# Kernel tuning notes

Hardware: AMD Instinct MI355X
Metric: run time of the kernel (lower is better)

The kernel has to match this reference:

```python
import jax, jax.numpy as jnp
import numpy as np

HIDDEN = 4096
NUM_HEADS = 32
HEAD_DIM = 128
NUM_KV_HEADS = 8
KV_GROUPS = NUM_HEADS // NUM_KV_HEADS
ROPE_THETA = 10000.0
SEQ = 2048
BATCH = 1
NEG_INF = -1e9


def fake_quant_int8(x):
    """Per-tensor symmetric int8 fake quantization (absmax scale)."""
    scale = jnp.maximum(jnp.max(jnp.abs(x)) / 127.0, 1e-8)
    q = jnp.clip(jnp.round(x / scale), -127.0, 127.0) * scale
    # straight-through estimator (no-op in fwd-only, keeps code shared)
    return x + jax.lax.stop_gradient(q - x)


def rotate_half(x):
    x1, x2 = jnp.split(x, 2, axis=-1)
    return jnp.concatenate([-x2, x1], axis=-1)


def rope_cos_sin(position_ids):
    inv_freq = 1.0 / (ROPE_THETA ** (jnp.arange(0, HEAD_DIM, 2, dtype=jnp.float32) / HEAD_DIM))
    freqs = position_ids.astype(jnp.float32)[..., None] * inv_freq  # [B,S,HD/2]
    emb = jnp.concatenate([freqs, freqs], axis=-1)                  # [B,S,HD]
    return jnp.cos(emb), jnp.sin(emb)


def setup_inputs() -> dict:
    key = jax.random.key(0)
    k1, k2, k3, k4, k5 = jax.random.split(key, 5)
    hidden_states = jax.random.normal(k1, (BATCH, SEQ, HIDDEN), dtype=jnp.float32)
    causal = jnp.tril(jnp.ones((SEQ, SEQ), dtype=bool))
    attention_mask = jnp.where(causal, 0.0, NEG_INF).astype(jnp.float32)[None, None]  # [1,1,S,S]
    position_ids = jnp.arange(SEQ, dtype=jnp.int64 if jax.config.jax_enable_x64 else jnp.int32)[None, :]
    s = 0.02
    wq = jax.random.normal(k2, (NUM_HEADS * HEAD_DIM, HIDDEN), dtype=jnp.float32) * s
    wk = jax.random.normal(k3, (NUM_KV_HEADS * HEAD_DIM, HIDDEN), dtype=jnp.float32) * s
    wv = jax.random.normal(k4, (NUM_KV_HEADS * HEAD_DIM, HIDDEN), dtype=jnp.float32) * s
    wo = jax.random.normal(k5, (HIDDEN, NUM_HEADS * HEAD_DIM), dtype=jnp.float32) * s
    return {"hidden_states": hidden_states, "attention_mask": attention_mask,
            "position_ids": position_ids, "wq": wq, "wk": wk, "wv": wv, "wo": wo}


def reference(hidden_states, attention_mask, position_ids, wq, wk, wv, wo):
    B, S, _ = hidden_states.shape

    def qlinear(x, w):  # quantized linear: fake-quant act and weight, y = x @ w.T
        return fake_quant_int8(x) @ fake_quant_int8(w).T

    q = qlinear(hidden_states, wq).reshape(B, S, NUM_HEADS, HEAD_DIM).transpose(0, 2, 1, 3)
    k = qlinear(hidden_states, wk).reshape(B, S, NUM_KV_HEADS, HEAD_DIM).transpose(0, 2, 1, 3)
    v = qlinear(hidden_states, wv).reshape(B, S, NUM_KV_HEADS, HEAD_DIM).transpose(0, 2, 1, 3)

    cos, sin = rope_cos_sin(position_ids)      # [B,S,HD]
    cos, sin = cos[:, None], sin[:, None]      # [B,1,S,HD]
    q = q * cos + rotate_half(q) * sin
    k = k * cos + rotate_half(k) * sin

    # repeat_kv: GQA -> full heads
    k = jnp.repeat(k, KV_GROUPS, axis=1)
    v = jnp.repeat(v, KV_GROUPS, axis=1)

    # quantized QK^T
    scores = jnp.einsum('bhqd,bhkd->bhqk', fake_quant_int8(q), fake_quant_int8(k))
    scores = scores * (1.0 / np.sqrt(HEAD_DIM).astype(np.float32))
    scores = scores + attention_mask[:, :, :, :S]
    probs = jax.nn.softmax(scores.astype(jnp.float32), axis=-1).astype(q.dtype)
    # attention_dropout = 0.0 -> identity

    # quantized AV
    attn_out = jnp.einsum('bhqk,bhkd->bhqd', fake_quant_int8(probs), fake_quant_int8(v))
    attn_out = attn_out.transpose(0, 2, 1, 3).reshape(B, S, NUM_HEADS * HEAD_DIM)
    return qlinear(attn_out, wo)
```

## Files before the change

### kernel.cpp

```cpp
#include <hip/hip_runtime.h>
#include <stdint.h>

#define SEQ   2048
#define HID   4096
#define NH    32
#define NKV   8
#define KVDIM 1024
#define KVCAT 2048

typedef int v4i __attribute__((ext_vector_type(4)));

#define VMCNT0 asm volatile("s_waitcnt vmcnt(0)" ::: "memory")

__device__ __forceinline__ void gload16(const void* g, void* l) {
    __builtin_amdgcn_global_load_lds(
        (const __attribute__((address_space(1))) void*)(uintptr_t)g,
        (__attribute__((address_space(3))) void*)(uintptr_t)l, 16, 0, 0);
}

__device__ __forceinline__ float slot_scale(const unsigned* slots, int slot) {
    return fmaxf(__uint_as_float(slots[slot << 5]) / 127.0f, 1e-8f);
}

__device__ __forceinline__ int q8v(float x, float s) {
    int v = (int)rintf(x / s);
    return v < -127 ? -127 : (v > 127 ? 127 : v);
}

__device__ __forceinline__ float fexp2(float x) {
    float r; asm("v_exp_f32 %0, %1" : "=v"(r) : "v"(x)); return r;
}

__device__ __forceinline__ float amax4(const float* __restrict__ p, long v) {
    float4 x = *(const float4*)(p + v * 4);
    return fmaxf(fmaxf(fabsf(x.x), fabsf(x.y)), fmaxf(fabsf(x.z), fabsf(x.w)));
}

__device__ __forceinline__ void block_amax_store(float m, float* part) {
    __shared__ float sm[4];
    int lane = threadIdx.x & 63, w = threadIdx.x >> 6;
    for (int off = 32; off; off >>= 1) m = fmaxf(m, __shfl_xor(m, off, 64));
    if (lane == 0) sm[w] = m;
    __syncthreads();
    if (threadIdx.x == 0)
        part[blockIdx.x] = fmaxf(fmaxf(sm[0], sm[1]), fmaxf(sm[2], sm[3]));
}

#define NV0 ((long)SEQ * HID / 4)
#define NV1 ((long)HID * HID / 4)
#define NV2 ((long)KVDIM * HID / 4)
__global__ void k_absmax5(const float* __restrict__ a0, const float* __restrict__ a1,
                          const float* __restrict__ a2, const float* __restrict__ a3,
                          const float* __restrict__ a4, float* __restrict__ part) {
    int b = blockIdx.x;
    const float* p; long n; int lb, nb;
    if (b < 342)       { p = a0; n = NV0; lb = b;        nb = 342; }
    else if (b < 1025) { p = a1; n = NV1; lb = b - 342;  nb = 683; }
    else if (b < 1196) { p = a2; n = NV2; lb = b - 1025; nb = 171; }
    else if (b < 1367) { p = a3; n = NV2; lb = b - 1196; nb = 171; }
    else               { p = a4; n = NV1; lb = b - 1367; nb = 681; }
    long str = (long)nb * 256;
    float mm[8] = {0.f, 0.f, 0.f, 0.f, 0.f, 0.f, 0.f, 0.f};
    long v = (long)lb * 256 + threadIdx.x;
    for (; v + 7 * str < n; v += 8 * str) {
        #pragma unroll
        for (int j = 0; j < 8; j++) mm[j] = fmaxf(mm[j], amax4(p, v + j * str));
    }
    for (; v < n; v += str) mm[0] = fmaxf(mm[0], amax4(p, v));
    float m = fmaxf(fmaxf(fmaxf(mm[0], mm[1]), fmaxf(mm[2], mm[3])),
                    fmaxf(fmaxf(mm[4], mm[5]), fmaxf(mm[6], mm[7])));
    block_amax_store(m, part);
}

__global__ void k_reduceA(const float* __restrict__ part, unsigned* slots) {
    __shared__ float sm[4];
    const int lo[5] = {0, 342, 1025, 1196, 1367};
    const int hi[5] = {342, 1025, 1196, 1367, 2048};
    int t = threadIdx.x, lane = t & 63, w = t >> 6;
    for (int s = 0; s < 5; s++) {
        float m = 0.f;
        for (int i = lo[s] + t; i < hi[s]; i += 256) m = fmaxf(m, part[i]);
        for (int off = 32; off; off >>= 1) m = fmaxf(m, __shfl_xor(m, off, 64));
        if (lane == 0) sm[w] = m;
        __syncthreads();
        if (t == 0)
            slots[s << 5] = __float_as_uint(fmaxf(fmaxf(sm[0], sm[1]), fmaxf(sm[2], sm[3])));
        __syncthreads();
    }
}

__global__ void k_reduceB(const float* __restrict__ p1, const float* __restrict__ p2,
                          const float* __restrict__ p3, unsigned* slots) {
    __shared__ float sm[4];
    int t = threadIdx.x, lane = t & 63, w = t >> 6;
    const float* ps[3] = {p1, p2, p3};
    const int cnt[3] = {2048, 1024, 256};
    const int sl[3] = {5, 6, 7};
    for (int s = 0; s < 3; s++) {
        float m = 0.f;
        for (int i = t; i < cnt[s]; i += 256) m = fmaxf(m, ps[s][i]);
        for (int off = 32; off; off >>= 1) m = fmaxf(m, __shfl_xor(m, off, 64));
        if (lane == 0) sm[w] = m;
        __syncthreads();
        if (t == 0)
            slots[sl[s] << 5] = __float_as_uint(fmaxf(fmaxf(sm[0], sm[1]), fmaxf(sm[2], sm[3])));
        __syncthreads();
    }
}

__device__ __forceinline__ void qstore4(const float* __restrict__ src, long v,
                                        int8_t* __restrict__ dst, float s) {
    float4 x = *(const float4*)(src + v * 4);
    unsigned pa = (unsigned)(uint8_t)(int8_t)q8v(x.x, s)
                | ((unsigned)(uint8_t)(int8_t)q8v(x.y, s) << 8)
                | ((unsigned)(uint8_t)(int8_t)q8v(x.z, s) << 16)
                | ((unsigned)(uint8_t)(int8_t)q8v(x.w, s) << 24);
    *(unsigned*)(dst + v * 4) = pa;
}

__global__ void k_quant4(const float* __restrict__ a0, const float* __restrict__ a1,
                         const float* __restrict__ a2, const float* __restrict__ a3,
                         int8_t* __restrict__ d0, int8_t* __restrict__ d1,
                         int8_t* __restrict__ d2, int8_t* __restrict__ d3,
                         const unsigned* __restrict__ slots) {
    int b = blockIdx.x;
    const float* p; int8_t* d; long n; int slot, lb, nb;
    if (b < 512)       { p = a0; d = d0; n = NV0; slot = 0; lb = b;        nb = 512; }
    else if (b < 1536) { p = a1; d = d1; n = NV1; slot = 1; lb = b - 512;  nb = 1024; }
    else if (b < 1792) { p = a2; d = d2; n = NV2; slot = 2; lb = b - 1536; nb = 256; }
    else               { p = a3; d = d3; n = NV2; slot = 3; lb = b - 1792; nb = 256; }
    float s = slot_scale(slots, slot);
    long str = (long)nb * 256;
    long v = (long)lb * 256 + threadIdx.x;
    for (; v + 3 * str < n; v += 4 * str) {
        #pragma unroll
        for (int j = 0; j < 4; j++) qstore4(p, v + j * str, d, s);
    }
    for (; v < n; v += str) qstore4(p, v, d, s);
}

__global__ void k_quant(const float* __restrict__ x, int8_t* __restrict__ q, long nvec,
                        int rshift, long cmaskv, long ld,
                        const unsigned* __restrict__ slots, int slot) {
    float s = slot_scale(slots, slot);
    long gs = (long)gridDim.x * blockDim.x;
    long v = blockIdx.x * (long)blockDim.x + threadIdx.x;
    for (; v + 3 * gs < nvec; v += 4 * gs) {
        #pragma unroll
        for (int j = 0; j < 4; j++) {
            long vid = v + j * gs;
            long r = vid >> rshift;
            long c = (vid & cmaskv) << 2;
            float4 vv = *(const float4*)(x + r * ld + c);
            unsigned pa = (unsigned)(uint8_t)(int8_t)q8v(vv.x, s)
                        | ((unsigned)(uint8_t)(int8_t)q8v(vv.y, s) << 8)
                        | ((unsigned)(uint8_t)(int8_t)q8v(vv.z, s) << 16)
                        | ((unsigned)(uint8_t)(int8_t)q8v(vv.w, s) << 24);
            *(unsigned*)(q + vid * 4) = pa;
        }
    }
    for (; v < nvec; v += gs) {
        long r = v >> rshift;
        long c = (v & cmaskv) << 2;
        float4 vv = *(const float4*)(x + r * ld + c);
        unsigned pa = (unsigned)(uint8_t)(int8_t)q8v(vv.x, s)
                    | ((unsigned)(uint8_t)(int8_t)q8v(vv.y, s) << 8)
                    | ((unsigned)(uint8_t)(int8_t)q8v(vv.z, s) << 16)
                    | ((unsigned)(uint8_t)(int8_t)q8v(vv.w, s) << 24);
        *(unsigned*)(q + v * 4) = pa;
    }
}

__global__ void k_ropetab(const int* __restrict__ pos, float* __restrict__ ct,
                          float* __restrict__ st) {
    int tid = blockIdx.x * blockDim.x + threadIdx.x;
    if (tid >= SEQ * 64) return;
    int i = tid & 63, s = tid >> 6;
    double inv = 1.0 / pow(10000.0, (double)((float)(2 * i) * (1.0f / 128.0f)));
    float invf = (float)inv;
    float angf = (float)pos[s] * invf;
    double a = (double)angf;
    ct[tid] = (float)cos(a);
    st[tid] = (float)sin(a);
}

__global__ void k_rope(float* __restrict__ x, long ld, int hbits, int total,
                       const float* __restrict__ ct, const float* __restrict__ st,
                       float* __restrict__ part) {
    float m = 0.f;
    for (int t = blockIdx.x * blockDim.x + threadIdx.x; t < total;
         t += gridDim.x * blockDim.x) {
        int i4 = t & 15;
        int h = (t >> 4) & ((1 << hbits) - 1);
        int s = t >> (4 + hbits);
        long base = (long)s * ld + h * 128 + i4 * 4;
        float4 a = *(float4*)(x + base);
        float4 b = *(float4*)(x + base + 64);
        float4 c = *(const float4*)(ct + s * 64 + i4 * 4);
        float4 sn = *(const float4*)(st + s * 64 + i4 * 4);
        float4 o0, o1;
        o0.x = a.x * c.x - b.x * sn.x;  o1.x = b.x * c.x + a.x * sn.x;
        o0.y = a.y * c.y - b.y * sn.y;  o1.y = b.y * c.y + a.y * sn.y;
        o0.z = a.z * c.z - b.z * sn.z;  o1.z = b.z * c.z + a.z * sn.z;
        o0.w = a.w * c.w - b.w * sn.w;  o1.w = b.w * c.w + a.w * sn.w;
        *(float4*)(x + base) = o0;
        *(float4*)(x + base + 64) = o1;
        m = fmaxf(m,
            fmaxf(fmaxf(fmaxf(fabsf(o0.x), fabsf(o0.y)), fmaxf(fabsf(o0.z), fabsf(o0.w))),
                  fmaxf(fmaxf(fabsf(o1.x), fabsf(o1.y)), fmaxf(fabsf(o1.z), fabsf(o1.w)))));
    }
    block_amax_store(m, part);
}

__global__ void k_transq(const float* __restrict__ src, long lds_, int8_t* __restrict__ dst,
                         long ldd, const unsigned* __restrict__ slots, int slot) {
    __shared__ float t[32][33];
    float s = slot_scale(slots, slot);
    int bx = blockIdx.x, by = blockIdx.y;
    int tid = threadIdx.x;
    int c = tid & 31, r0 = tid >> 5;
    #pragma unroll
    for (int j = 0; j < 4; j++) {
        int r = r0 + j * 8;
        t[r][c] = src[(long)(by * 32 + r) * lds_ + bx * 32 + c];
    }
    __syncthreads();
    int d = tid >> 3, k4 = (tid & 7) * 4;
    unsigned pa = 0;
    #pragma unroll
    for (int j = 0; j < 4; j++) {
        int iv = q8v(t[k4 + j][d], s);
        pa |= ((unsigned)(uint8_t)(int8_t)iv) << (8 * j);
    }
    *(unsigned*)(dst + (long)(bx * 32 + d) * ldd + by * 32 + k4) = pa;
}

__global__ __launch_bounds__(256) void k_gemm_i8(
    const int8_t* __restrict__ A, const int8_t* __restrict__ B, float* __restrict__ C,
    int M, int N, int K, unsigned* slots,
    int slotA, int slotB, int slotB2, int nsplit, float* am_part, int am_col0) {
    __shared__ int8_t As[2][128 * 128];
    __shared__ int8_t Bs[2][128 * 128];
    const v4i vzero = {0, 0, 0, 0};
    int tid = threadIdx.x, lane = tid & 63, wid = tid >> 6;
    int nbx = N >> 7;
    int nwg = gridDim.x, wg = blockIdx.x;
    int cpx = nwg >> 3;
    int swz = (wg & 7) * cpx + (wg >> 3);
    int bm = swz / nbx, bn = swz % nbx;
    long rowA0 = (long)bm * 128, colB0 = (long)bn * 128;
    int wrow = (wid >> 1) * 64, wcol = (wid & 1) * 64;
    int lr = lane >> 3;
    int swc = ((lane & 7) ^ lr) * 16;
    const int8_t* ga = A + (rowA0 + wid * 8 + lr) * (long)K + swc;
    const int8_t* gb = B + (colB0 + wid * 8 + lr) * (long)K + swc;
    v4i acc[4][4];
    #pragma unroll
    for (int m = 0; m < 4; m++)
        #pragma unroll
        for (int n = 0; n < 4; n++) acc[m][n] = vzero;

    auto STAGE = [&](int buf, int kt) {
        #pragma unroll
        for (int i = 0; i < 4; i++) {
            gload16(ga + kt + (long)(i * 32) * K, &As[buf][(wid * 8 + i * 32) * 128]);
            gload16(gb + kt + (long)(i * 32) * K, &Bs[buf][(wid * 8 + i * 32) * 128]);
        }
    };
    auto COMPUTE = [&](int buf) {
        #pragma unroll
        for (int ks = 0; ks < 2; ks++) {
            v4i af[4], bf[4];
            #pragma unroll
            for (int m = 0; m < 4; m++) {
                int row = wrow + m * 16 + (lane & 15);
                af[m] = *(const v4i*)(&As[buf][row * 128 + (((ks * 4 + (lane >> 4)) ^ (row & 7)) * 16)]);
            }
            #pragma unroll
            for (int n = 0; n < 4; n++) {
                int row = wcol + n * 16 + (lane & 15);
                bf[n] = *(const v4i*)(&Bs[buf][row * 128 + (((ks * 4 + (lane >> 4)) ^ (row & 7)) * 16)]);
            }
            #pragma unroll
            for (int m = 0; m < 4; m++)
                #pragma unroll
                for (int n = 0; n < 4; n++)
                    acc[m][n] = __builtin_amdgcn_mfma_i32_16x16x64_i8(af[m], bf[n], acc[m][n], 0, 0, 0);
        }
    };

    STAGE(0, 0);
    VMCNT0;
    __syncthreads();
    int nt = K >> 7, cur = 0;
    for (int t = 0; t < nt - 1; t++) {
        STAGE(cur ^ 1, (t + 1) << 7);
        COMPUTE(cur);
        VMCNT0;
        __syncthreads();
        cur ^= 1;
    }
    COMPUTE(cur);

    float sA = slot_scale(slots, slotA);
    float sB1 = slot_scale(slots, slotB);
    float sB2 = slot_scale(slots, slotB2);
    float am = 0.f;
    #pragma unroll
    for (int m = 0; m < 4; m++) {
        long row0 = rowA0 + wrow + m * 16 + ((lane >> 4) << 2);
        #pragma unroll
        for (int n = 0; n < 4; n++) {
            int col = (int)colB0 + wcol + n * 16 + (lane & 15);
            float sc = sA * ((col < nsplit) ? sB1 : sB2);
            float* cp = C + row0 * N + col;
            #pragma unroll
            for (int r = 0; r < 4; r++) {
                float val = sc * (float)acc[m][n][r];
                cp[(long)r * N] = val;
                if (col >= am_col0) am = fmaxf(am, fabsf(val));
            }
        }
    }
    if (am_part) block_amax_store(am, am_part);
}

__global__ __launch_bounds__(256) void k_attn(
    const int8_t* __restrict__ Qq, const int8_t* __restrict__ Kq, const int8_t* __restrict__ Vtq,
    int* __restrict__ AO, unsigned* slots) {
    __shared__ int8_t Qs[64 * 128];
    __shared__ int8_t Ks[2][64 * 128];
    __shared__ int8_t Vs[2][128 * 64];
    __shared__ int smx[4];
    const v4i vzero = {0, 0, 0, 0};
    const int NEGS = -(1 << 29);
    int tid = threadIdx.x, lane = tid & 63, w = tid >> 6;
    int qlan = lane & 15, g = lane >> 4;
    int idx = blockIdx.x;
    int qb = 31 - (idx >> 5), h = idx & 31, kvh = h >> 2;
    float sq = slot_scale(slots, 5), sk = slot_scale(slots, 6);
    float c2 = sq * sk * 0.08838834764831845f * 1.4426950408889634f;
    int lr8 = lane >> 3;
    int swc = ((lane & 7) ^ lr8) * 16;
    int lr4 = lane >> 2;
    int vswc = ((lane & 3) ^ (lr4 & 3)) * 16;
    const int8_t* kbase = Kq + ((long)(w * 8 + lr8)) * KVDIM + kvh * 128 + swc;
    const int8_t* vbase = Vtq + ((long)kvh * 128 + w * 16 + lr4) * SEQ + vswc;
    auto STAGE_K = [&](int buf, int kt) {
        #pragma unroll
        for (int i = 0; i < 2; i++)
            gload16(kbase + ((long)kt * 64 + i * 32) * KVDIM, &Ks[buf][(w * 8 + i * 32) * 128]);
    };
    auto STAGE_V = [&](int buf, int kt) {
        #pragma unroll
        for (int i = 0; i < 2; i++)
            gload16(vbase + (long)(i * 64) * SEQ + kt * 64, &Vs[buf][(w * 16 + i * 64) * 64]);
    };
    {
        const int8_t* qbase = Qq + ((long)qb * 64 + w * 8 + lr8) * HID + h * 128 + swc;
        #pragma unroll
        for (int i = 0; i < 2; i++)
            gload16(qbase + (long)(i * 32) * HID, &Qs[(w * 8 + i * 32) * 128]);
    }
    STAGE_K(0, 0);
    VMCNT0;
    __syncthreads();
    v4i aq[2];
    #pragma unroll
    for (int ks = 0; ks < 2; ks++) {
        int row = w * 16 + qlan;
        aq[ks] = *(const v4i*)(&Qs[row * 128 + (((ks * 4 + g) ^ (row & 7)) * 16)]);
    }
    int mi = -(1 << 30);
    float l = 0.f;
    int buf = 0;
    for (int kt = 0; kt <= qb; kt++) {
        if (kt < qb) STAGE_K(buf ^ 1, kt + 1);
        v4i sf[4] = {vzero, vzero, vzero, vzero};
        __builtin_amdgcn_s_setprio(1);
        #pragma unroll
        for (int ks = 0; ks < 2; ks++)
            #pragma unroll
            for (int f = 0; f < 4; f++) {
                int row = f * 16 + qlan;
                v4i bk = *(const v4i*)(&Ks[buf][row * 128 + (((ks * 4 + g) ^ (row & 7)) * 16)]);
                sf[f] = __builtin_amdgcn_mfma_i32_16x16x64_i8(bk, aq[ks], sf[f], 0, 0, 0);
            }
        __builtin_amdgcn_s_setprio(0);
        int sv[16];
        if (kt == qb) {
            int qthr = w * 16 + qlan;
            #pragma unroll
            for (int f = 0; f < 4; f++)
                #pragma unroll
                for (int r = 0; r < 4; r++) {
                    int kl = f * 16 + g * 4 + r;
                    sv[f * 4 + r] = (kl > qthr) ? NEGS : sf[f][r];
                }
        } else {
            #pragma unroll
            for (int f = 0; f < 4; f++)
                #pragma unroll
                for (int r = 0; r < 4; r++) sv[f * 4 + r] = sf[f][r];
        }
        int tm = sv[0];
        #pragma unroll
        for (int e = 1; e < 16; e++) tm = tm > sv[e] ? tm : sv[e];
        tm = max(tm, __shfl_xor(tm, 16, 64));
        tm = max(tm, __shfl_xor(tm, 32, 64));
        int mn = tm > mi ? tm : mi;
        float esc = fexp2(c2 * (float)(mi - mn));
        float es = 0.f;
        #pragma unroll
        for (int e = 0; e < 16; e++) es += fexp2(c2 * (float)(sv[e] - mn));
        es += __shfl_xor(es, 16, 64);
        es += __shfl_xor(es, 32, 64);
        l = l * esc + es;
        mi = mn;
        VMCNT0;
        __syncthreads();
        buf ^= 1;
    }
    float invl = 127.0f / l;
    unsigned* Ps32 = (unsigned*)Qs;
    int pwr = w * 320;
    v4i of[8];
    #pragma unroll
    for (int nf = 0; nf < 8; nf++) of[nf] = vzero;
    STAGE_K(0, 0);
    STAGE_V(0, 0);
    VMCNT0;
    __syncthreads();
    buf = 0;
    for (int kt = 0; kt <= qb; kt++) {
        if (kt < qb) { STAGE_K(buf ^ 1, kt + 1); STAGE_V(buf ^ 1, kt + 1); }
        v4i sf[4] = {vzero, vzero, vzero, vzero};
        __builtin_amdgcn_s_setprio(1);
        #pragma unroll
        for (int ks = 0; ks < 2; ks++)
            #pragma unroll
            for (int f = 0; f < 4; f++) {
                int row = f * 16 + qlan;
                v4i bk = *(const v4i*)(&Ks[buf][row * 128 + (((ks * 4 + g) ^ (row & 7)) * 16)]);
                sf[f] = __builtin_amdgcn_mfma_i32_16x16x64_i8(bk, aq[ks], sf[f], 0, 0, 0);
            }
        __builtin_amdgcn_s_setprio(0);
        if (kt == qb) {
            int qthr = w * 16 + qlan;
            #pragma unroll
            for (int f = 0; f < 4; f++) {
                unsigned pk = 0;
                #pragma unroll
                for (int r = 0; r < 4; r++) {
                    int kl = f * 16 + g * 4 + r;
                    int s = (kl > qthr) ? NEGS : sf[f][r];
                    float t = fexp2(c2 * (float)(s - mi));
                    int pq = (int)rintf(t * invl);
                    pk |= ((unsigned)pq) << (8 * r);
                }
                Ps32[pwr + (4 * f + g) * 20 + qlan] = pk;
            }
        } else {
            #pragma unroll
            for (int f = 0; f < 4; f++) {
                unsigned pk = 0;
                #pragma unroll
                for (int r = 0; r < 4; r++) {
                    float t = fexp2(c2 * (float)(sf[f][r] - mi));
                    int pq = (int)rintf(t * invl);
                    pk |= ((unsigned)pq) << (8 * r);
                }
                Ps32[pwr + (4 * f + g) * 20 + qlan] = pk;
            }
        }
        int rb = pwr + 80 * g + qlan;
        v4i ap;
        ap[0] = (int)Ps32[rb];
        ap[1] = (int)Ps32[rb + 20];
        ap[2] = (int)Ps32[rb + 40];
        ap[3] = (int)Ps32[rb + 60];
        __builtin_amdgcn_s_setprio(1);
        #pragma unroll
        for (int nf = 0; nf < 8; nf++) {
            int row = nf * 16 + qlan;
            v4i bv = *(const v4i*)(&Vs[buf][row * 64 + ((g ^ (row & 3)) * 16)]);
            of[nf] = __builtin_amdgcn_mfma_i32_16x16x64_i8(ap, bv, of[nf], 0, 0, 0);
        }
        __builtin_amdgcn_s_setprio(0);
        VMCNT0;
        __syncthreads();
        buf ^= 1;
    }
    int mymax = 0;
    #pragma unroll
    for (int nf = 0; nf < 8; nf++)
        #pragma unroll
        for (int r = 0; r < 4; r++) {
            int val = of[nf][r];
            int av = val < 0 ? -val : val;
            mymax = av > mymax ? av : mymax;
            int qg = qb * 64 + w * 16 + 4 * g + r;
            AO[(long)qg * HID + h * 128 + nf * 16 + qlan] = val;
        }
    #pragma unroll
    for (int off = 1; off < 64; off <<= 1) {
        int o2 = __shfl_xor(mymax, off, 64);
        mymax = o2 > mymax ? o2 : mymax;
    }
    if (lane == 0) smx[w] = mymax;
    __syncthreads();
    if (tid == 0) {
        int mm = max(max(smx[0], smx[1]), max(smx[2], smx[3]));
        atomicMax(slots + (8 << 5), (unsigned)mm);
    }
}

__global__ void k_quant_ao(const int* __restrict__ a, int8_t* __restrict__ q, unsigned* slots) {
    float sv = slot_scale(slots, 7);
    float spv = (1.0f / 127.0f) * sv;
    float amax = spv * (float)(int)slots[8 << 5];
    float s = fmaxf(amax / 127.0f, 1e-8f);
    long nvec = (long)SEQ * HID / 4;
    long gs = (long)gridDim.x * blockDim.x;
    long v = blockIdx.x * (long)blockDim.x + threadIdx.x;
    for (; v + 3 * gs < nvec; v += 4 * gs) {
        #pragma unroll
        for (int j = 0; j < 4; j++) {
            long vid = v + j * gs;
            int4 x = *(const int4*)(a + vid * 4);
            int a0 = q8v(spv * (float)x.x, s);
            int a1 = q8v(spv * (float)x.y, s);
            int a2 = q8v(spv * (float)x.z, s);
            int a3 = q8v(spv * (float)x.w, s);
            unsigned pa = (unsigned)(uint8_t)(int8_t)a0
                        | ((unsigned)(uint8_t)(int8_t)a1 << 8)
                        | ((unsigned)(uint8_t)(int8_t)a2 << 16)
                        | ((unsigned)(uint8_t)(int8_t)a3 << 24);
            *(unsigned*)(q + vid * 4) = pa;
        }
    }
    for (; v < nvec; v += gs) {
        int4 x = *(const int4*)(a + v * 4);
        int a0 = q8v(spv * (float)x.x, s);
        int a1 = q8v(spv * (float)x.y, s);
        int a2 = q8v(spv * (float)x.z, s);
        int a3 = q8v(spv * (float)x.w, s);
        unsigned pa = (unsigned)(uint8_t)(int8_t)a0
                    | ((unsigned)(uint8_t)(int8_t)a1 << 8)
                    | ((unsigned)(uint8_t)(int8_t)a2 << 16)
                    | ((unsigned)(uint8_t)(int8_t)a3 << 24);
        *(unsigned*)(q + v * 4) = pa;
    }
    if (blockIdx.x == 0 && threadIdx.x == 0) slots[9 << 5] = __float_as_uint(amax);
}

extern "C" void kernel_launch(void* const* d_in, const int* in_sizes, int n_in,
                              void* d_out, int out_size, void* d_ws, size_t ws_size,
                              hipStream_t stream) {
    (void)in_sizes; (void)n_in; (void)out_size;
    const float* hid = (const float*)d_in[0];
    const int* pos = (const int*)d_in[2];
    const float* wqp = (const float*)d_in[3];
    const float* wkp = (const float*)d_in[4];
    const float* wvp = (const float*)d_in[5];
    const float* wop = (const float*)d_in[6];
    float* out = (float*)d_out;
    char* ws = (char*)d_ws;

    size_t o = 0;
    auto alloc = [&](size_t sz) { size_t r = o; o += (sz + 255) & ~(size_t)255; return r; };
    unsigned* slots = (unsigned*)(ws + alloc(2048));
    float* P0 = (float*)(ws + alloc(2048 * 4));
    float* P1 = (float*)(ws + alloc(2048 * 4));
    float* P2 = (float*)(ws + alloc(1024 * 4));
    float* P3 = (float*)(ws + alloc(256 * 4));
    int8_t* Xq   = (int8_t*)(ws + alloc((size_t)SEQ * HID));
    int8_t* Wqq  = (int8_t*)(ws + alloc((size_t)HID * HID));
    int8_t* Wkvq = (int8_t*)(ws + alloc((size_t)KVCAT * HID));
    float*  Qf   = (float*)(ws + alloc((size_t)SEQ * HID * 4));
    float*  KVf  = (float*)(ws + alloc((size_t)SEQ * KVCAT * 4));
    int8_t* Qq   = (int8_t*)(ws + alloc((size_t)SEQ * HID));
    int8_t* Kq   = (int8_t*)(ws + alloc((size_t)SEQ * KVDIM));
    int8_t* Vtq  = (int8_t*)(ws + alloc((size_t)KVDIM * SEQ));
    float*  ctab = (float*)(ws + alloc((size_t)SEQ * 64 * 4));
    float*  stab = (float*)(ws + alloc((size_t)SEQ * 64 * 4));
    if (ws_size < o) return;
    int8_t* Woq = Wqq;
    int*    AOint = (int*)Qf;
    int8_t* AOq = Xq;

    hipMemsetAsync(slots, 0, 2048, stream);
    k_ropetab<<<SEQ * 64 / 256, 256, 0, stream>>>(pos, ctab, stab);
    k_absmax5<<<2048, 256, 0, stream>>>(hid, wqp, wkp, wvp, wop, P0);
    k_reduceA<<<1, 256, 0, stream>>>(P0, slots);
    k_quant4<<<2048, 256, 0, stream>>>(hid, wqp, wkp, wvp,
                                       Xq, Wqq, Wkvq, Wkvq + (size_t)KVDIM * HID, slots);
    k_gemm_i8<<<512, 256, 0, stream>>>(Xq, Wqq, Qf, SEQ, HID, HID, slots,
                                       0, 1, 1, 1 << 30, nullptr, 1 << 30);
    k_gemm_i8<<<256, 256, 0, stream>>>(Xq, Wkvq, KVf, SEQ, KVCAT, HID, slots,
                                       0, 2, 3, KVDIM, P3, KVDIM);
    const long CALL = 0x3FFFFFFFL;
    k_quant<<<2048, 256, 0, stream>>>(wop, Woq, (long)HID * HID / 4, 40, CALL, 0, slots, 4);
    k_rope<<<2048, 256, 0, stream>>>(Qf, HID, 5, SEQ * NH * 16, ctab, stab, P1);
    k_rope<<<1024, 256, 0, stream>>>(KVf, KVCAT, 3, SEQ * NKV * 16, ctab, stab, P2);
    k_reduceB<<<1, 256, 0, stream>>>(P1, P2, P3, slots);
    k_quant<<<2048, 256, 0, stream>>>(Qf, Qq, (long)SEQ * HID / 4, 40, CALL, 0, slots, 5);
    k_quant<<<512, 256, 0, stream>>>(KVf, Kq, (long)SEQ * KVDIM / 4, 8, 255, KVCAT, slots, 6);
    k_transq<<<dim3(32, 64), 256, 0, stream>>>(KVf + KVDIM, KVCAT, Vtq, SEQ, slots, 7);
    k_attn<<<1024, 256, 0, stream>>>(Qq, Kq, Vtq, AOint, slots);
    k_quant_ao<<<2048, 256, 0, stream>>>(AOint, AOq, slots);
    k_gemm_i8<<<512, 256, 0, stream>>>(AOq, Woq, out, SEQ, HID, HID, slots,
                                       9, 4, 4, 1 << 30, nullptr, 1 << 30);
}
```

Measured before the change: 312.6 us.

## Fuse RoPE and absmax into GEMM epilogue, restage absmax and attention loads

The RoPE rotation and its absmax partials now run inside the Q and KV GEMM epilogues through an LDS exchange buffer, which removes the two standalone k_rope passes over Qf and KVf. The absmax kernel now stages 16 KB chunks into LDS with global_load_lds double buffering and writes per-tensor partials. The attention kernel drops its double-buffered LDS K/V and instead prefetches the next tile into registers, adding two barriers per iteration. This frees LDS, but it risks exposing load latency and adding sync cost inside attention.

```diff
diff --git a/kernel.cpp b/kernel.cpp
--- a/kernel.cpp
+++ b/kernel.cpp
@@ -31,59 +31,66 @@
     float r; asm("v_exp_f32 %0, %1" : "=v"(r) : "v"(x)); return r;
 }
 
-__device__ __forceinline__ float amax4(const float* __restrict__ p, long v) {
-    float4 x = *(const float4*)(p + v * 4);
-    return fmaxf(fmaxf(fabsf(x.x), fabsf(x.y)), fmaxf(fabsf(x.z), fabsf(x.w)));
-}
-
-__device__ __forceinline__ void block_amax_store(float m, float* part) {
+__device__ __forceinline__ void block_amax_part(float m, float* dst) {
     __shared__ float sm[4];
     int lane = threadIdx.x & 63, w = threadIdx.x >> 6;
     for (int off = 32; off; off >>= 1) m = fmaxf(m, __shfl_xor(m, off, 64));
     if (lane == 0) sm[w] = m;
     __syncthreads();
     if (threadIdx.x == 0)
-        part[blockIdx.x] = fmaxf(fmaxf(sm[0], sm[1]), fmaxf(sm[2], sm[3]));
-}
-
-#define NV0 ((long)SEQ * HID / 4)
-#define NV1 ((long)HID * HID / 4)
-#define NV2 ((long)KVDIM * HID / 4)
-__global__ void k_absmax5(const float* __restrict__ a0, const float* __restrict__ a1,
-                          const float* __restrict__ a2, const float* __restrict__ a3,
-                          const float* __restrict__ a4, float* __restrict__ part) {
-    int b = blockIdx.x;
-    const float* p; long n; int lb, nb;
-    if (b < 342)       { p = a0; n = NV0; lb = b;        nb = 342; }
-    else if (b < 1025) { p = a1; n = NV1; lb = b - 342;  nb = 683; }
-    else if (b < 1196) { p = a2; n = NV2; lb = b - 1025; nb = 171; }
-    else if (b < 1367) { p = a3; n = NV2; lb = b - 1196; nb = 171; }
-    else               { p = a4; n = NV1; lb = b - 1367; nb = 681; }
-    long str = (long)nb * 256;
-    float mm[8] = {0.f, 0.f, 0.f, 0.f, 0.f, 0.f, 0.f, 0.f};
-    long v = (long)lb * 256 + threadIdx.x;
-    for (; v + 7 * str < n; v += 8 * str) {
-        #pragma unroll
-        for (int j = 0; j < 8; j++) mm[j] = fmaxf(mm[j], amax4(p, v + j * str));
-    }
-    for (; v < n; v += str) mm[0] = fmaxf(mm[0], amax4(p, v));
-    float m = fmaxf(fmaxf(fmaxf(mm[0], mm[1]), fmaxf(mm[2], mm[3])),
-                    fmaxf(fmaxf(mm[4], mm[5]), fmaxf(mm[6], mm[7])));
-    block_amax_store(m, part);
+        *dst = fmaxf(fmaxf(sm[0], sm[1]), fmaxf(sm[2], sm[3]));
+    __syncthreads();
+}
+
+__global__ __launch_bounds__(256) void k_absmax5(
+    const float* __restrict__ a0, const float* __restrict__ a1,
+    const float* __restrict__ a2, const float* __restrict__ a3,
+    const float* __restrict__ a4, float* __restrict__ part) {
+    __shared__ int8_t SB[4][2][4096];
+    int lane = threadIdx.x & 63, w = threadIdx.x >> 6;
+    const char* bases[5] = {(const char*)a0, (const char*)a1, (const char*)a2,
+                            (const char*)a3, (const char*)a4};
+    const int lo[5] = {0, 2048, 6144, 7168, 8192};
+    float m[5] = {0.f, 0.f, 0.f, 0.f, 0.f};
+    int u0 = blockIdx.x * 12;
+    auto tensor_of = [&](int u) {
+        return (u < 2048) ? 0 : (u < 6144) ? 1 : (u < 7168) ? 2 : (u < 8192) ? 3 : 4; };
+    auto stage = [&](int u, int buf) {
+        int t = tensor_of(u);
+        const char* s = bases[t] + ((long)(u - lo[t]) << 14) + w * 4096 + lane * 16;
+        #pragma unroll
+        for (int i = 0; i < 4; i++) gload16(s + i * 1024, &SB[w][buf][i * 1024]);
+    };
+    stage(u0, 0);
+    for (int j = 0; j < 12; j++) {
+        if (j < 11) {
+            stage(u0 + j + 1, (j + 1) & 1);
+            asm volatile("s_waitcnt vmcnt(4)" ::: "memory");
+        } else {
+            asm volatile("s_waitcnt vmcnt(0)" ::: "memory");
+        }
+        int t = tensor_of(u0 + j);
+        #pragma unroll
+        for (int i = 0; i < 4; i++) {
+            float4 v = *(const float4*)&SB[w][j & 1][i * 1024 + lane * 16];
+            m[t] = fmaxf(m[t],
+                fmaxf(fmaxf(fabsf(v.x), fabsf(v.y)), fmaxf(fabsf(v.z), fabsf(v.w))));
+        }
+    }
+    __syncthreads();
+    for (int t = 0; t < 5; t++) block_amax_part(m[t], part + t * 1024 + blockIdx.x);
 }
 
 __global__ void k_reduceA(const float* __restrict__ part, unsigned* slots) {
     __shared__ float sm[4];
-    const int lo[5] = {0, 342, 1025, 1196, 1367};
-    const int hi[5] = {342, 1025, 1196, 1367, 2048};
-    int t = threadIdx.x, lane = t & 63, w = t >> 6;
+    int t0 = threadIdx.x, lane = t0 & 63, w = t0 >> 6;
     for (int s = 0; s < 5; s++) {
         float m = 0.f;
-        for (int i = lo[s] + t; i < hi[s]; i += 256) m = fmaxf(m, part[i]);
+        for (int i = t0; i < 1024; i += 256) m = fmaxf(m, part[s * 1024 + i]);
         for (int off = 32; off; off >>= 1) m = fmaxf(m, __shfl_xor(m, off, 64));
         if (lane == 0) sm[w] = m;
         __syncthreads();
-        if (t == 0)
+        if (t0 == 0)
             slots[s << 5] = __float_as_uint(fmaxf(fmaxf(sm[0], sm[1]), fmaxf(sm[2], sm[3])));
         __syncthreads();
     }
@@ -92,17 +99,17 @@
 __global__ void k_reduceB(const float* __restrict__ p1, const float* __restrict__ p2,
                           const float* __restrict__ p3, unsigned* slots) {
     __shared__ float sm[4];
-    int t = threadIdx.x, lane = t & 63, w = t >> 6;
+    int t0 = threadIdx.x, lane = t0 & 63, w = t0 >> 6;
     const float* ps[3] = {p1, p2, p3};
-    const int cnt[3] = {2048, 1024, 256};
+    const int cnt[3] = {512, 128, 128};
     const int sl[3] = {5, 6, 7};
     for (int s = 0; s < 3; s++) {
         float m = 0.f;
-        for (int i = t; i < cnt[s]; i += 256) m = fmaxf(m, ps[s][i]);
+        for (int i = t0; i < cnt[s]; i += 256) m = fmaxf(m, ps[s][i]);
         for (int off = 32; off; off >>= 1) m = fmaxf(m, __shfl_xor(m, off, 64));
         if (lane == 0) sm[w] = m;
         __syncthreads();
-        if (t == 0)
+        if (t0 == 0)
             slots[sl[s] << 5] = __float_as_uint(fmaxf(fmaxf(sm[0], sm[1]), fmaxf(sm[2], sm[3])));
         __syncthreads();
     }
@@ -118,6 +125,9 @@
     *(unsigned*)(dst + v * 4) = pa;
 }
 
+#define NV0 ((long)SEQ * HID / 4)
+#define NV1 ((long)HID * HID / 4)
+#define NV2 ((long)KVDIM * HID / 4)
 __global__ void k_quant4(const float* __restrict__ a0, const float* __restrict__ a1,
                          const float* __restrict__ a2, const float* __restrict__ a3,
                          int8_t* __restrict__ d0, int8_t* __restrict__ d1,
@@ -184,34 +194,6 @@
     st[tid] = (float)sin(a);
 }
 
-__global__ void k_rope(float* __restrict__ x, long ld, int hbits, int total,
-                       const float* __restrict__ ct, const float* __restrict__ st,
-                       float* __restrict__ part) {
-    float m = 0.f;
-    for (int t = blockIdx.x * blockDim.x + threadIdx.x; t < total;
-         t += gridDim.x * blockDim.x) {
-        int i4 = t & 15;
-        int h = (t >> 4) & ((1 << hbits) - 1);
-        int s = t >> (4 + hbits);
-        long base = (long)s * ld + h * 128 + i4 * 4;
-        float4 a = *(float4*)(x + base);
-        float4 b = *(float4*)(x + base + 64);
-        float4 c = *(const float4*)(ct + s * 64 + i4 * 4);
-        float4 sn = *(const float4*)(st + s * 64 + i4 * 4);
-        float4 o0, o1;
-        o0.x = a.x * c.x - b.x * sn.x;  o1.x = b.x * c.x + a.x * sn.x;
-        o0.y = a.y * c.y - b.y * sn.y;  o1.y = b.y * c.y + a.y * sn.y;
-        o0.z = a.z * c.z - b.z * sn.z;  o1.z = b.z * c.z + a.z * sn.z;
-        o0.w = a.w * c.w - b.w * sn.w;  o1.w = b.w * c.w + a.w * sn.w;
-        *(float4*)(x + base) = o0;
-        *(float4*)(x + base + 64) = o1;
-        m = fmaxf(m,
-            fmaxf(fmaxf(fmaxf(fabsf(o0.x), fabsf(o0.y)), fmaxf(fabsf(o0.z), fabsf(o0.w))),
-                  fmaxf(fmaxf(fabsf(o1.x), fabsf(o1.y)), fmaxf(fabsf(o1.z), fabsf(o1.w)))));
-    }
-    block_amax_store(m, part);
-}
-
 __global__ void k_transq(const float* __restrict__ src, long lds_, int8_t* __restrict__ dst,
                          long ldd, const unsigned* __restrict__ slots, int slot) {
     __shared__ float t[32][33];
@@ -238,9 +220,12 @@
 __global__ __launch_bounds__(256) void k_gemm_i8(
     const int8_t* __restrict__ A, const int8_t* __restrict__ B, float* __restrict__ C,
     int M, int N, int K, unsigned* slots,
-    int slotA, int slotB, int slotB2, int nsplit, float* am_part, int am_col0) {
-    __shared__ int8_t As[2][128 * 128];
-    __shared__ int8_t Bs[2][128 * 128];
+    int slotA, int slotB, int slotB2, int nsplit,
+    float* pQ, float* pK, float* pV, int ropemode,
+    const float* __restrict__ ct, const float* __restrict__ st) {
+    __shared__ int8_t POOL[65536];
+    int8_t (*As)[16384] = (int8_t(*)[16384])POOL;
+    int8_t (*Bs)[16384] = (int8_t(*)[16384])(POOL + 32768);
     const v4i vzero = {0, 0, 0, 0};
     int tid = threadIdx.x, lane = tid & 63, wid = tid >> 6;
     int nbx = N >> 7;
@@ -305,32 +290,83 @@
     float sA = slot_scale(slots, slotA);
     float sB1 = slot_scale(slots, slotB);
     float sB2 = slot_scale(slots, slotB2);
-    float am = 0.f;
-    #pragma unroll
-    for (int m = 0; m < 4; m++) {
-        long row0 = rowA0 + wrow + m * 16 + ((lane >> 4) << 2);
-        #pragma unroll
-        for (int n = 0; n < 4; n++) {
-            int col = (int)colB0 + wcol + n * 16 + (lane & 15);
-            float sc = sA * ((col < nsplit) ? sB1 : sB2);
-            float* cp = C + row0 * N + col;
-            #pragma unroll
-            for (int r = 0; r < 4; r++) {
-                float val = sc * (float)acc[m][n][r];
-                cp[(long)r * N] = val;
-                if (col >= am_col0) am = fmaxf(am, fabsf(val));
-            }
-        }
-    }
-    if (am_part) block_amax_store(am, am_part);
+    int qc = lane & 15, rgrp = (lane >> 4) << 2;
+    if (ropemode == 1 || (ropemode == 2 && bn < 8)) {
+        __syncthreads();
+        float* EX = (float*)POOL;
+        #pragma unroll
+        for (int m = 0; m < 4; m++)
+            #pragma unroll
+            for (int n = 0; n < 4; n++) {
+                int coll = wcol + n * 16 + qc;
+                #pragma unroll
+                for (int r = 0; r < 4; r++) {
+                    int rowl = wrow + m * 16 + rgrp + r;
+                    EX[rowl * 128 + (coll ^ ((rowl & 1) << 4))] = sA * sB1 * (float)acc[m][n][r];
+                }
+            }
+        __syncthreads();
+        float am = 0.f;
+        #pragma unroll
+        for (int m = 0; m < 4; m++)
+            #pragma unroll
+            for (int n = 0; n < 4; n++) {
+                int coll = wcol + n * 16 + qc;
+                #pragma unroll
+                for (int r = 0; r < 4; r++) {
+                    int rowl = wrow + m * 16 + rgrp + r;
+                    long srow = rowA0 + rowl;
+                    float self = EX[rowl * 128 + (coll ^ ((rowl & 1) << 4))];
+                    float pv = EX[rowl * 128 + ((coll ^ 64) ^ ((rowl & 1) << 4))];
+                    float c = ct[srow * 64 + (coll & 63)];
+                    float sn = st[srow * 64 + (coll & 63)];
+                    float o = (coll < 64) ? self * c - pv * sn : self * c + pv * sn;
+                    am = fmaxf(am, fabsf(o));
+                    C[srow * N + colB0 + coll] = o;
+                }
+            }
+        block_amax_part(am, (ropemode == 1) ? pQ + blockIdx.x : pK + bm * 8 + (bn & 7));
+    } else if (ropemode == 2) {
+        float am = 0.f;
+        #pragma unroll
+        for (int m = 0; m < 4; m++) {
+            long row0 = rowA0 + wrow + m * 16 + rgrp;
+            #pragma unroll
+            for (int n = 0; n < 4; n++) {
+                int col = (int)colB0 + wcol + n * 16 + qc;
+                float sc = sA * ((col < nsplit) ? sB1 : sB2);
+                float* cp = C + row0 * N + col;
+                #pragma unroll
+                for (int r = 0; r < 4; r++) {
+                    float val = sc * (float)acc[m][n][r];
+                    cp[(long)r * N] = val;
+                    am = fmaxf(am, fabsf(val));
+                }
+            }
+        }
+        block_amax_part(am, pV + bm * 8 + (bn & 7));
+    } else {
+        #pragma unroll
+        for (int m = 0; m < 4; m++) {
+            long row0 = rowA0 + wrow + m * 16 + rgrp;
+            #pragma unroll
+            for (int n = 0; n < 4; n++) {
+                int col = (int)colB0 + wcol + n * 16 + qc;
+                float sc = sA * ((col < nsplit) ? sB1 : sB2);
+                float* cp = C + row0 * N + col;
+                #pragma unroll
+                for (int r = 0; r < 4; r++) cp[(long)r * N] = sc * (float)acc[m][n][r];
+            }
+        }
+    }
 }
 
 __global__ __launch_bounds__(256) void k_attn(
     const int8_t* __restrict__ Qq, const int8_t* __restrict__ Kq, const int8_t* __restrict__ Vtq,
     int* __restrict__ AO, unsigned* slots) {
     __shared__ int8_t Qs[64 * 128];
-    __shared__ int8_t Ks[2][64 * 128];
-    __shared__ int8_t Vs[2][128 * 64];
+    __shared__ int8_t Ks[64 * 128];
+    __shared__ int8_t Vs[128 * 64];
     __shared__ int smx[4];
     const v4i vzero = {0, 0, 0, 0};
     const int NEGS = -(1 << 29);
@@ -346,23 +382,22 @@
     int vswc = ((lane & 3) ^ (lr4 & 3)) * 16;
     const int8_t* kbase = Kq + ((long)(w * 8 + lr8)) * KVDIM + kvh * 128 + swc;
     const int8_t* vbase = Vtq + ((long)kvh * 128 + w * 16 + lr4) * SEQ + vswc;
-    auto STAGE_K = [&](int buf, int kt) {
-        #pragma unroll
-        for (int i = 0; i < 2; i++)
-            gload16(kbase + ((long)kt * 64 + i * 32) * KVDIM, &Ks[buf][(w * 8 + i * 32) * 128]);
+    int kds0 = (w * 8) * 128 + lane * 16,  kds1 = (w * 8 + 32) * 128 + lane * 16;
+    int vds0 = (w * 16) * 64 + lane * 16,  vds1 = (w * 16 + 64) * 64 + lane * 16;
+    auto STAGE_K_g = [&](int kt) {
+        gload16(kbase + ((long)kt * 64) * KVDIM, &Ks[(w * 8) * 128]);
+        gload16(kbase + ((long)kt * 64 + 32) * KVDIM, &Ks[(w * 8 + 32) * 128]);
     };
-    auto STAGE_V = [&](int buf, int kt) {
-        #pragma unroll
-        for (int i = 0; i < 2; i++)
-            gload16(vbase + (long)(i * 64) * SEQ + kt * 64, &Vs[buf][(w * 16 + i * 64) * 64]);
+    auto STAGE_V_g = [&](int kt) {
+        gload16(vbase + kt * 64, &Vs[(w * 16) * 64]);
+        gload16(vbase + (long)64 * SEQ + kt * 64, &Vs[(w * 16 + 64) * 64]);
     };
     {
         const int8_t* qbase = Qq + ((long)qb * 64 + w * 8 + lr8) * HID + h * 128 + swc;
-        #pragma unroll
-        for (int i = 0; i < 2; i++)
-            gload16(qbase + (long)(i * 32) * HID, &Qs[(w * 8 + i * 32) * 128]);
-    }
-    STAGE_K(0, 0);
+        gload16(qbase, &Qs[(w * 8) * 128]);
+        gload16(qbase + (long)32 * HID, &Qs[(w * 8 + 32) * 128]);
+    }
+    STAGE_K_g(0);
     VMCNT0;
     __syncthreads();
     v4i aq[2];
@@ -373,9 +408,13 @@
     }
     int mi = -(1 << 30);
     float l = 0.f;
-    int buf = 0;
     for (int kt = 0; kt <= qb; kt++) {
-        if (kt < qb) STAGE_K(buf ^ 1, kt + 1);
+        bool pf = kt < qb;
+        v4i kr0, kr1;
+        if (pf) {
+            kr0 = *(const v4i*)(kbase + ((long)(kt + 1) * 64) * KVDIM);
+            kr1 = *(const v4i*)(kbase + ((long)(kt + 1) * 64 + 32) * KVDIM);
+        }
         v4i sf[4] = {vzero, vzero, vzero, vzero};
         __builtin_amdgcn_s_setprio(1);
         #pragma unroll
@@ -383,7 +422,7 @@
             #pragma unroll
             for (int f = 0; f < 4; f++) {
                 int row = f * 16 + qlan;
-                v4i bk = *(const v4i*)(&Ks[buf][row * 128 + (((ks * 4 + g) ^ (row & 7)) * 16)]);
+                v4i bk = *(const v4i*)(&Ks[row * 128 + (((ks * 4 + g) ^ (row & 7)) * 16)]);
                 sf[f] = __builtin_amdgcn_mfma_i32_16x16x64_i8(bk, aq[ks], sf[f], 0, 0, 0);
             }
         __builtin_amdgcn_s_setprio(0);
@@ -417,9 +456,12 @@
         es += __shfl_xor(es, 32, 64);
         l = l * esc + es;
         mi = mn;
-        VMCNT0;
-        __syncthreads();
-        buf ^= 1;
+        if (pf) {
+            __syncthreads();
+            *(v4i*)&Ks[kds0] = kr0;
+            *(v4i*)&Ks[kds1] = kr1;
+            __syncthreads();
+        }
     }
     float invl = 127.0f / l;
     unsigned* Ps32 = (unsigned*)Qs;
@@ -427,13 +469,20 @@
     v4i of[8];
     #pragma unroll
     for (int nf = 0; nf < 8; nf++) of[nf] = vzero;
-    STAGE_K(0, 0);
-    STAGE_V(0, 0);
+    __syncthreads();
+    STAGE_K_g(0);
+    STAGE_V_g(0);
     VMCNT0;
     __syncthreads();
-    buf = 0;
     for (int kt = 0; kt <= qb; kt++) {
-        if (kt < qb) { STAGE_K(buf ^ 1, kt + 1); STAGE_V(buf ^ 1, kt + 1); }
+        bool pf = kt < qb;
+        v4i kr0, kr1, vr0, vr1;
+        if (pf) {
+            kr0 = *(const v4i*)(kbase + ((long)(kt + 1) * 64) * KVDIM);
+            kr1 = *(const v4i*)(kbase + ((long)(kt + 1) * 64 + 32) * KVDIM);
+            vr0 = *(const v4i*)(vbase + (kt + 1) * 64);
+            vr1 = *(const v4i*)(vbase + (long)64 * SEQ + (kt + 1) * 64);
+        }
         v4i sf[4] = {vzero, vzero, vzero, vzero};
         __builtin_amdgcn_s_setprio(1);
         #pragma unroll
@@ -441,7 +490,7 @@
             #pragma unroll
             for (int f = 0; f < 4; f++) {
                 int row = f * 16 + qlan;
-                v4i bk = *(const v4i*)(&Ks[buf][row * 128 + (((ks * 4 + g) ^ (row & 7)) * 16)]);
+                v4i bk = *(const v4i*)(&Ks[row * 128 + (((ks * 4 + g) ^ (row & 7)) * 16)]);
                 sf[f] = __builtin_amdgcn_mfma_i32_16x16x64_i8(bk, aq[ks], sf[f], 0, 0, 0);
             }
         __builtin_amdgcn_s_setprio(0);
@@ -483,13 +532,18 @@
         #pragma unroll
         for (int nf = 0; nf < 8; nf++) {
             int row = nf * 16 + qlan;
-            v4i bv = *(const v4i*)(&Vs[buf][row * 64 + ((g ^ (row & 3)) * 16)]);
+            v4i bv = *(const v4i*)(&Vs[row * 64 + ((g ^ (row & 3)) * 16)]);
             of[nf] = __builtin_amdgcn_mfma_i32_16x16x64_i8(ap, bv, of[nf], 0, 0, 0);
         }
         __builtin_amdgcn_s_setprio(0);
-        VMCNT0;
-        __syncthreads();
-        buf ^= 1;
+        if (pf) {
+            __syncthreads();
+            *(v4i*)&Ks[kds0] = kr0;
+            *(v4i*)&Ks[kds1] = kr1;
+            *(v4i*)&Vs[vds0] = vr0;
+            *(v4i*)&Vs[vds1] = vr1;
+            __syncthreads();
+        }
     }
     int mymax = 0;
     #pragma unroll
@@ -570,10 +624,10 @@
     size_t o = 0;
     auto alloc = [&](size_t sz) { size_t r = o; o += (sz + 255) & ~(size_t)255; return r; };
     unsigned* slots = (unsigned*)(ws + alloc(2048));
-    float* P0 = (float*)(ws + alloc(2048 * 4));
-    float* P1 = (float*)(ws + alloc(2048 * 4));
-    float* P2 = (float*)(ws + alloc(1024 * 4));
-    float* P3 = (float*)(ws + alloc(256 * 4));
+    float* P0 = (float*)(ws + alloc(5 * 1024 * 4));
+    float* P1 = (float*)(ws + alloc(512 * 4));
+    float* P2 = (float*)(ws + alloc(128 * 4));
+    float* P3 = (float*)(ws + alloc(128 * 4));
     int8_t* Xq   = (int8_t*)(ws + alloc((size_t)SEQ * HID));
     int8_t* Wqq  = (int8_t*)(ws + alloc((size_t)HID * HID));
     int8_t* Wkvq = (int8_t*)(ws + alloc((size_t)KVCAT * HID));
@@ -591,18 +645,16 @@
 
     hipMemsetAsync(slots, 0, 2048, stream);
     k_ropetab<<<SEQ * 64 / 256, 256, 0, stream>>>(pos, ctab, stab);
-    k_absmax5<<<2048, 256, 0, stream>>>(hid, wqp, wkp, wvp, wop, P0);
+    k_absmax5<<<1024, 256, 0, stream>>>(hid, wqp, wkp, wvp, wop, P0);
     k_reduceA<<<1, 256, 0, stream>>>(P0, slots);
     k_quant4<<<2048, 256, 0, stream>>>(hid, wqp, wkp, wvp,
                                        Xq, Wqq, Wkvq, Wkvq + (size_t)KVDIM * HID, slots);
     k_gemm_i8<<<512, 256, 0, stream>>>(Xq, Wqq, Qf, SEQ, HID, HID, slots,
-                                       0, 1, 1, 1 << 30, nullptr, 1 << 30);
+                                       0, 1, 1, 1 << 30, P1, nullptr, nullptr, 1, ctab, stab);
     k_gemm_i8<<<256, 256, 0, stream>>>(Xq, Wkvq, KVf, SEQ, KVCAT, HID, slots,
-                                       0, 2, 3, KVDIM, P3, KVDIM);
+                                       0, 2, 3, KVDIM, nullptr, P2, P3, 2, ctab, stab);
     const long CALL = 0x3FFFFFFFL;
     k_quant<<<2048, 256, 0, stream>>>(wop, Woq, (long)HID * HID / 4, 40, CALL, 0, slots, 4);
-    k_rope<<<2048, 256, 0, stream>>>(Qf, HID, 5, SEQ * NH * 16, ctab, stab, P1);
-    k_rope<<<1024, 256, 0, stream>>>(KVf, KVCAT, 3, SEQ * NKV * 16, ctab, stab, P2);
     k_reduceB<<<1, 256, 0, stream>>>(P1, P2, P3, slots);
     k_quant<<<2048, 256, 0, stream>>>(Qf, Qq, (long)SEQ * HID / 4, 40, CALL, 0, slots, 5);
     k_quant<<<512, 256, 0, stream>>>(KVf, Kq, (long)SEQ * KVDIM / 4, 8, 255, KVCAT, slots, 6);
@@ -610,5 +662,6 @@
     k_attn<<<1024, 256, 0, stream>>>(Qq, Kq, Vtq, AOint, slots);
     k_quant_ao<<<2048, 256, 0, stream>>>(AOint, AOq, slots);
     k_gemm_i8<<<512, 256, 0, stream>>>(AOq, Woq, out, SEQ, HID, HID, slots,
-                                       9, 4, 4, 1 << 30, nullptr, 1 << 30);
-}
+                                       9, 4, 4, 1 << 30, nullptr, nullptr, nullptr, 0,
+                                       nullptr, nullptr);
+}
```

After: 310.0 us. No clear change (-0.8%).
